# Kernel tuning notes

Measured on AMD Instinct MI355X. Metric: run time of the kernel, lower is better.

## Reference

```python
import jax, jax.numpy as jnp
import numpy as np

BB, F, K, D, H, HFF, L, M_PREV = 128, 8, 256, 256, 256, 512, 2, 2


def setup_inputs() -> dict:
    key = jax.random.key(0)
    ks = jax.random.split(key, 16)
    f32 = jnp.float32

    def lin(k, fan_in, shape):
        return (jax.random.normal(k, shape, dtype=f32) / np.sqrt(fan_in)).astype(f32)

    inp = {
        "x_BD": jax.random.normal(ks[0], (BB, D), dtype=f32),
        "xhat_BFD": jax.random.normal(ks[1], (BB, F, D), dtype=f32),
        "codes_MBF": jax.random.randint(ks[2], (M_PREV, BB, 1), 0, F * K, dtype=jnp.int64),
        "codebook": jax.random.normal(ks[3], (K, D), dtype=f32) / np.sqrt(D),
        "W_in": lin(ks[4], D, (D, H)),
        "b_in": jnp.zeros((H,), f32),
        # concat projection over cat([h, xhat], -1): (H + D) -> H
        "W_cat": lin(ks[5], H + D, (H + D, H)),
        "b_cat": jnp.zeros((H,), f32),
        "W1": lin(ks[6], H, (L, H, HFF)),
        "b1": jnp.zeros((L, HFF), f32),
        "W2": lin(ks[7], HFF, (L, HFF, H)),
        "b2": jnp.zeros((L, H), f32),
        "W_out": lin(ks[8], H, (H, D)),
        "b_out": jnp.zeros((D,), f32),
    }
    return inp


def reference(x_BD, xhat_BFD, codes_MBF, codebook, W_in, b_in, W_cat, b_cat,
              W1, b1, W2, b2, W_out, b_out):
    Bb, Fb, Dd = xhat_BFD.shape
    Kk = codebook.shape[0]

    # in_proj applied to the (shared) codebook once: [K, H]
    h0 = codebook @ W_in + b_in

    # concat(h, xhat) as a linear over the concatenation, split to avoid
    # materializing a [Bb,F,K,H+D] tensor.
    Wc, Wx = W_cat[:H], W_cat[H:]
    h = (h0 @ Wc)[None, None] + (xhat_BFD @ Wx)[:, :, None] + b_cat  # [Bb,F,K,H]

    # residual MLP blocks: h <- h + W2 relu(W1 h)
    for l in range(L):
        h = h + jax.nn.relu(h @ W1[l] + b1[l]) @ W2[l] + b2[l]

    # out_proj + residual codeword (res_codeword_coeff = 1.0) + xhat offset
    cw = h @ W_out + b_out + codebook[None, None]        # [Bb,F,K,D]
    cw = cw + xhat_BFD[:, :, None]                        # reconstructed candidates

    cflat = cw.reshape(Bb, Fb * Kk, Dd)                   # [Bb, F*K, D]

    dists = (jnp.sum(x_BD * x_BD, -1, keepdims=True)
             - 2.0 * jnp.einsum('bd,bkd->bk', x_BD, cflat)
             + jnp.sum(cflat * cflat, -1))                # [Bb, F*K]

    idx = jnp.argmin(dists, axis=-1)                      # [Bb]
    xhat_next_BFD = jnp.take_along_axis(cflat, idx[:, None, None], axis=1)  # [Bb,1,D]

    codes_new = jnp.concatenate(
        [codes_MBF, idx[None, :, None].astype(codes_MBF.dtype)], axis=0)
    return xhat_next_BFD, codes_new
```

## Files before the change

### kernel.cpp

```cpp
#include <hip/hip_runtime.h>
#include <hip/hip_bf16.h>

#define B_   128
#define F_   8
#define K_   256
#define D_   256
#define H_   256
#define HFF_ 512
#define RT   64

typedef _Float16 half8  __attribute__((ext_vector_type(8)));
typedef _Float16 half4v __attribute__((ext_vector_type(4)));
typedef float floatx4   __attribute__((ext_vector_type(4)));

#define MFMAH(a,b,c) __builtin_amdgcn_mfma_f32_16x16x32_f16(a,b,c,0,0,0)

#define HA_S  260
#define HMA_S 132

__global__ void k_prep(const float* __restrict__ cb, const float* __restrict__ Win,
                       const float* __restrict__ bin, const float* __restrict__ Wcat,
                       const float* __restrict__ bcat, const float* __restrict__ xhat,
                       const float* __restrict__ W1, const float* __restrict__ W2,
                       const float* __restrict__ Wout,
                       float* __restrict__ u, float* __restrict__ v,
                       _Float16* __restrict__ w1f, _Float16* __restrict__ w2f,
                       _Float16* __restrict__ wof) {
  const int blk = blockIdx.x, t = threadIdx.x;
  if (blk < K_) {
    __shared__ float row[D_];
    __shared__ float h0row[H_];
    row[t] = cb[blk * D_ + t];
    __syncthreads();
    float acc = bin[t];
    #pragma unroll 4
    for (int i = 0; i < D_; ++i) acc = fmaf(row[i], Win[i * H_ + t], acc);
    h0row[t] = acc;
    __syncthreads();
    float acc2 = 0.f;
    #pragma unroll 4
    for (int i = 0; i < H_; ++i) acc2 = fmaf(h0row[i], Wcat[i * H_ + t], acc2);
    u[blk * H_ + t] = acc2;
  } else if (blk < K_ + B_ * F_) {
    __shared__ float row2[D_];
    const int bf = blk - K_;
    row2[t] = xhat[bf * D_ + t];
    __syncthreads();
    float acc = bcat[t];
    #pragma unroll 4
    for (int i = 0; i < D_; ++i) acc = fmaf(row2[i], Wcat[(H_ + i) * H_ + t], acc);
    v[bf * H_ + t] = acc;
  } else {
    const int e = (blk - (K_ + B_ * F_)) * 256 + t;
    const float* src; _Float16* dst; int N, NT, le;
    if (e < 262144) {
      const int layer = e >> 17; le = e & 131071;
      src = W1 + layer * (H_ * HFF_); dst = w1f + layer * (H_ * HFF_);
      N = HFF_; NT = 32;
    } else if (e < 524288) {
      const int e2 = e - 262144;
      const int layer = e2 >> 17; le = e2 & 131071;
      src = W2 + layer * (HFF_ * H_); dst = w2f + layer * (HFF_ * H_);
      N = H_; NT = 16;
    } else {
      le = e - 524288; src = Wout; dst = wof; N = D_; NT = 16;
    }
    const int jj = le & 7, lane = (le >> 3) & 63, r = le >> 9;
    const int ntile = r % NT, kstep = r / NT;
    const int row = kstep * 32 + (lane >> 4) * 8 + jj;
    const int colc = ntile * 16 + (lane & 15);
    dst[le] = (_Float16)src[row * N + colc];
  }
}

__global__ __launch_bounds__(256, 3) void k_main(
    const float* __restrict__ u, const float* __restrict__ v,
    const _Float16* __restrict__ w1f, const float* __restrict__ b1,
    const _Float16* __restrict__ w2f, const float* __restrict__ b2,
    const _Float16* __restrict__ woutf, const float* __restrict__ bout,
    const float* __restrict__ cb, const float* __restrict__ xhat,
    const float* __restrict__ x, float* __restrict__ dists) {
  __shared__ _Float16 hA[64][HA_S];
  __shared__ _Float16 hmA[64][HMA_S];
  __shared__ float x_s[D_], xh_s[D_];
  __shared__ float dist_s[4][64];

  const int t = threadIdx.x;
  const int blk = blockIdx.x;
  const int bf = blk >> 2, k0 = (blk & 3) << 6;
  const int b = bf >> 3, f = bf & 7;
  const int wave = t >> 6, lane = t & 63;
  const int col = lane & 15, quad = lane >> 4;
  const int lane8 = lane * 8;

  x_s[t]  = x[b * D_ + t];
  xh_s[t] = xhat[bf * D_ + t];

  {
    const int r = t >> 2, c0 = (t & 3) * 64;
    const float* up = u + (k0 + r) * H_ + c0;
    const float* vp = v + bf * H_ + c0;
    #pragma unroll
    for (int j = 0; j < 64; j += 8) {
      float4 uA = *(const float4*)(up + j);
      float4 vA = *(const float4*)(vp + j);
      float4 uB = *(const float4*)(up + j + 4);
      float4 vB = *(const float4*)(vp + j + 4);
      half8 hv8;
      hv8[0] = (_Float16)(uA.x + vA.x); hv8[1] = (_Float16)(uA.y + vA.y);
      hv8[2] = (_Float16)(uA.z + vA.z); hv8[3] = (_Float16)(uA.w + vA.w);
      hv8[4] = (_Float16)(uB.x + vB.x); hv8[5] = (_Float16)(uB.y + vB.y);
      hv8[6] = (_Float16)(uB.z + vB.z); hv8[7] = (_Float16)(uB.w + vB.w);
      *(half8*)&hA[r][c0 + j] = hv8;
    }
  }
  __syncthreads();

  const floatx4 zero4 = {0.f, 0.f, 0.f, 0.f};

  #pragma unroll 1
  for (int l = 0; l < 2; ++l) {
    const _Float16* w1_l = w1f + l * (H_ * HFF_);
    const _Float16* w2_l = w2f + l * (HFF_ * H_);
    const float* b1l = b1 + l * HFF_;
    const float* b2l = b2 + l * H_;

    floatx4 acc2[4][4];
    #pragma unroll
    for (int mt = 0; mt < 4; ++mt)
      #pragma unroll
      for (int nt = 0; nt < 4; ++nt) acc2[mt][nt] = zero4;

    #pragma unroll 1
    for (int ch = 0; ch < 4; ++ch) {
      floatx4 acc1[2][4];
      #pragma unroll
      for (int mt = 0; mt < 2; ++mt)
        #pragma unroll
        for (int nt = 0; nt < 4; ++nt) acc1[mt][nt] = zero4;

      const _Float16* w1_b = w1_l + (ch * 8 + wave * 2) * 512 + lane8;

      #pragma unroll 4
      for (int ks = 0; ks < 8; ++ks) {
        half8 b0 = *(const half8*)&hA[col][ks * 32 + quad * 8];
        half8 b1v = *(const half8*)&hA[16 + col][ks * 32 + quad * 8];
        half8 b2v = *(const half8*)&hA[32 + col][ks * 32 + quad * 8];
        half8 b3v = *(const half8*)&hA[48 + col][ks * 32 + quad * 8];
        const int ko = ks * 32 * 512;
        #pragma unroll
        for (int mt = 0; mt < 2; ++mt) {
          half8 aw = *(const half8*)(w1_b + ko + mt * 512);
          acc1[mt][0] = MFMAH(aw, b0, acc1[mt][0]);
          acc1[mt][1] = MFMAH(aw, b1v, acc1[mt][1]);
          acc1[mt][2] = MFMAH(aw, b2v, acc1[mt][2]);
          acc1[mt][3] = MFMAH(aw, b3v, acc1[mt][3]);
        }
      }
      #pragma unroll
      for (int mt = 0; mt < 2; ++mt) {
        const int floc = (wave * 2 + mt) * 16 + quad * 4;
        float4 bb = *(const float4*)&b1l[ch * 128 + floc];
        #pragma unroll
        for (int nt = 0; nt < 4; ++nt) {
          const int row = nt * 16 + col;
          half4v nh;
          #pragma unroll
          for (int p = 0; p < 4; ++p)
            nh[p] = (_Float16)fmaxf(acc1[mt][nt][p] + ((const float*)&bb)[p], 0.f);
          *(half4v*)&hmA[row][floc] = nh;
        }
      }
      __syncthreads();

      const _Float16* w2_b = w2_l + (ch * 64 + wave * 4) * 512 + lane8;
      #pragma unroll 2
      for (int ks = 0; ks < 4; ++ks) {
        half8 b0 = *(const half8*)&hmA[col][ks * 32 + quad * 8];
        half8 b1v = *(const half8*)&hmA[16 + col][ks * 32 + quad * 8];
        half8 b2v = *(const half8*)&hmA[32 + col][ks * 32 + quad * 8];
        half8 b3v = *(const half8*)&hmA[48 + col][ks * 32 + quad * 8];
        const int ko = ks * 16 * 512;
        #pragma unroll
        for (int mt = 0; mt < 4; ++mt) {
          half8 aw = *(const half8*)(w2_b + ko + mt * 512);
          acc2[mt][0] = MFMAH(aw, b0, acc2[mt][0]);
          acc2[mt][1] = MFMAH(aw, b1v, acc2[mt][1]);
          acc2[mt][2] = MFMAH(aw, b2v, acc2[mt][2]);
          acc2[mt][3] = MFMAH(aw, b3v, acc2[mt][3]);
        }
      }
      __syncthreads();
    }

    #pragma unroll
    for (int mt = 0; mt < 4; ++mt) {
      const int feat0 = (wave * 4 + mt) * 16 + quad * 4;
      float4 bb = *(const float4*)&b2l[feat0];
      #pragma unroll
      for (int nt = 0; nt < 4; ++nt) {
        const int row = nt * 16 + col;
        half4v oh = *(half4v*)&hA[row][feat0];
        half4v nh;
        #pragma unroll
        for (int p = 0; p < 4; ++p)
          nh[p] = (_Float16)((float)oh[p] + acc2[mt][nt][p] + ((const float*)&bb)[p]);
        *(half4v*)&hA[row][feat0] = nh;
      }
    }
    __syncthreads();
  }

  floatx4 acc3[4][4];
  #pragma unroll
  for (int mt = 0; mt < 4; ++mt)
    #pragma unroll
    for (int nt = 0; nt < 4; ++nt) acc3[mt][nt] = zero4;

  const _Float16* wo_b = woutf + (wave * 4) * 512 + lane8;
  #pragma unroll 2
  for (int ks = 0; ks < 8; ++ks) {
    half8 b0 = *(const half8*)&hA[col][ks * 32 + quad * 8];
    half8 b1v = *(const half8*)&hA[16 + col][ks * 32 + quad * 8];
    half8 b2v = *(const half8*)&hA[32 + col][ks * 32 + quad * 8];
    half8 b3v = *(const half8*)&hA[48 + col][ks * 32 + quad * 8];
    const int ko = ks * 16 * 512;
    #pragma unroll
    for (int mt = 0; mt < 4; ++mt) {
      half8 aw = *(const half8*)(wo_b + ko + mt * 512);
      acc3[mt][0] = MFMAH(aw, b0, acc3[mt][0]);
      acc3[mt][1] = MFMAH(aw, b1v, acc3[mt][1]);
      acc3[mt][2] = MFMAH(aw, b2v, acc3[mt][2]);
      acc3[mt][3] = MFMAH(aw, b3v, acc3[mt][3]);
    }
  }

  float s[4] = {0.f, 0.f, 0.f, 0.f};
  #pragma unroll
  for (int mt = 0; mt < 4; ++mt) {
    const int d0 = (wave * 4 + mt) * 16 + quad * 4;
    float4 bo = *(const float4*)&bout[d0];
    float4 xv = *(const float4*)&x_s[d0];
    float4 xh4 = *(const float4*)&xh_s[d0];
    #pragma unroll
    for (int nt = 0; nt < 4; ++nt) {
      float4 cbv = *(const float4*)&cb[(k0 + nt * 16 + col) * D_ + d0];
      #pragma unroll
      for (int p = 0; p < 4; ++p) {
        float base = ((const float*)&bo)[p] + ((const float*)&xh4)[p];
        float xx = ((const float*)&xv)[p];
        float cw = acc3[mt][nt][p] + base + ((const float*)&cbv)[p];
        s[nt] += cw * (cw - 2.f * xx);
      }
    }
  }
  #pragma unroll
  for (int nt = 0; nt < 4; ++nt) {
    s[nt] += __shfl_xor(s[nt], 16, 64);
    s[nt] += __shfl_xor(s[nt], 32, 64);
  }
  if (quad == 0) {
    #pragma unroll
    for (int nt = 0; nt < 4; ++nt)
      dist_s[wave][nt * 16 + col] = s[nt];
  }
  __syncthreads();
  if (t < 64) {
    float d = dist_s[0][t] + dist_s[1][t] + dist_s[2][t] + dist_s[3][t];
    dists[b * (F_ * K_) + f * K_ + k0 + t] = d;
  }
}

__global__ void k_top8(const float* __restrict__ dists, int* __restrict__ topi) {
  __shared__ float ds[F_ * K_];
  __shared__ float bv[256];
  __shared__ int bi_s[256];
  const int b = blockIdx.x, t = threadIdx.x;
  for (int j = t; j < F_ * K_; j += 256) ds[j] = dists[b * (F_ * K_) + j];
  __syncthreads();
  for (int pass = 0; pass < 8; ++pass) {
    float best = 3.4e38f; int bi = 0;
    for (int j = t; j < F_ * K_; j += 256) {
      const float dv = ds[j];
      if (dv < best) { best = dv; bi = j; }
    }
    bv[t] = best; bi_s[t] = bi;
    __syncthreads();
    for (int s = 128; s > 0; s >>= 1) {
      if (t < s) {
        const float ov = bv[t + s]; const int oi = bi_s[t + s];
        if (ov < bv[t] || (ov == bv[t] && oi < bi_s[t])) { bv[t] = ov; bi_s[t] = oi; }
      }
      __syncthreads();
    }
    if (t == 0) { topi[b * 8 + pass] = bi_s[0]; ds[bi_s[0]] = 3.4e38f; }
    __syncthreads();
  }
}

__global__ void k_rescore(const float* __restrict__ u, const float* __restrict__ v,
                          const float* __restrict__ W1, const float* __restrict__ b1,
                          const float* __restrict__ W2, const float* __restrict__ b2,
                          const float* __restrict__ Wout, const float* __restrict__ bout,
                          const float* __restrict__ cb, const float* __restrict__ xhat,
                          const float* __restrict__ x, const int* __restrict__ topi,
                          float* __restrict__ resc) {
  __shared__ float hs[H_];
  __shared__ float hms[HFF_];
  __shared__ float red[256];
  const int bc = blockIdx.x, t = threadIdx.x;
  const int b = bc >> 3;
  const int idx = topi[bc];
  const int f = idx >> 8, k = idx & 255;
  const int bf = b * F_ + f;

  hs[t] = u[k * H_ + t] + v[bf * H_ + t];
  __syncthreads();
  for (int l = 0; l < 2; ++l) {
    const float* W1l = W1 + l * (H_ * HFF_);
    const float* W2l = W2 + l * (HFF_ * H_);
    float a0 = b1[l * HFF_ + t], a1 = b1[l * HFF_ + 256 + t];
    for (int i = 0; i < H_; ++i) {
      const float hv = hs[i];
      a0 = fmaf(hv, W1l[i * HFF_ + t], a0);
      a1 = fmaf(hv, W1l[i * HFF_ + 256 + t], a1);
    }
    hms[t] = fmaxf(a0, 0.f);
    hms[t + 256] = fmaxf(a1, 0.f);
    __syncthreads();
    float hn = hs[t] + b2[l * H_ + t];
    for (int jj = 0; jj < HFF_; ++jj)
      hn = fmaf(hms[jj], W2l[jj * H_ + t], hn);
    __syncthreads();
    hs[t] = hn;
    __syncthreads();
  }
  float cw = bout[t] + cb[k * D_ + t] + xhat[bf * D_ + t];
  for (int i = 0; i < H_; ++i) cw = fmaf(hs[i], Wout[i * D_ + t], cw);
  red[t] = cw * (cw - 2.f * x[b * D_ + t]);
  __syncthreads();
  for (int s = 128; s > 0; s >>= 1) {
    if (t < s) red[t] += red[t + s];
    __syncthreads();
  }
  if (t == 0) resc[bc] = red[0];
}

__global__ void k_final(const float* __restrict__ u, const float* __restrict__ v,
                        const float* __restrict__ W1, const float* __restrict__ b1,
                        const float* __restrict__ W2, const float* __restrict__ b2,
                        const float* __restrict__ Wout, const float* __restrict__ bout,
                        const float* __restrict__ cb, const float* __restrict__ xhat,
                        const int* __restrict__ codes, const int* __restrict__ topi,
                        const float* __restrict__ resc, float* __restrict__ out) {
  __shared__ float hs[H_];
  __shared__ float hms[HFF_];
  __shared__ int idx_sh;
  const int b = blockIdx.x, t = threadIdx.x;
  if (t == 0) {
    float bd = 3.4e38f; int bidx = 1 << 30;
    for (int c = 0; c < 8; ++c) {
      const float d = resc[b * 8 + c];
      const int ix = topi[b * 8 + c];
      if (d < bd || (d == bd && ix < bidx)) { bd = d; bidx = ix; }
    }
    idx_sh = bidx;
  }
  __syncthreads();
  const int idx = idx_sh;
  const int f = idx >> 8, k = idx & 255;
  const int bf = b * F_ + f;

  hs[t] = u[k * H_ + t] + v[bf * H_ + t];
  __syncthreads();
  for (int l = 0; l < 2; ++l) {
    const float* W1l = W1 + l * (H_ * HFF_);
    const float* W2l = W2 + l * (HFF_ * H_);
    float a0 = b1[l * HFF_ + t], a1 = b1[l * HFF_ + 256 + t];
    for (int i = 0; i < H_; ++i) {
      const float hv = hs[i];
      a0 = fmaf(hv, W1l[i * HFF_ + t], a0);
      a1 = fmaf(hv, W1l[i * HFF_ + 256 + t], a1);
    }
    hms[t] = fmaxf(a0, 0.f);
    hms[t + 256] = fmaxf(a1, 0.f);
    __syncthreads();
    float hn = hs[t] + b2[l * H_ + t];
    for (int jj = 0; jj < HFF_; ++jj)
      hn = fmaf(hms[jj], W2l[jj * H_ + t], hn);
    __syncthreads();
    hs[t] = hn;
    __syncthreads();
  }
  float cw = bout[t] + cb[k * D_ + t] + xhat[bf * D_ + t];
  for (int i = 0; i < H_; ++i) cw = fmaf(hs[i], Wout[i * D_ + t], cw);

  out[b * D_ + t] = cw;
  if (t < 2)
    out[B_ * D_ + t * B_ + b] = (float)codes[t * B_ + b];
  else if (t == 2)
    out[B_ * D_ + 2 * B_ + b] = (float)idx;
}

extern "C" void kernel_launch(void* const* d_in, const int* in_sizes, int n_in,
                              void* d_out, int out_size, void* d_ws, size_t ws_size,
                              hipStream_t stream) {
  const float* x    = (const float*)d_in[0];
  const float* xhat = (const float*)d_in[1];
  const int*   codes= (const int*)d_in[2];
  const float* cb   = (const float*)d_in[3];
  const float* Win  = (const float*)d_in[4];
  const float* bin  = (const float*)d_in[5];
  const float* Wcat = (const float*)d_in[6];
  const float* bcat = (const float*)d_in[7];
  const float* W1   = (const float*)d_in[8];
  const float* b1   = (const float*)d_in[9];
  const float* W2   = (const float*)d_in[10];
  const float* b2   = (const float*)d_in[11];
  const float* Wout = (const float*)d_in[12];
  const float* bout = (const float*)d_in[13];
  float* out = (float*)d_out;

  float* u     = (float*)d_ws;
  float* v     = u + K_ * H_;
  float* dists = v + B_ * F_ * H_;
  float* resc  = dists + B_ * F_ * K_;
  int*   topi  = (int*)(resc + 1024);
  int*   pad   = topi + 1024;
  _Float16* w1f  = (_Float16*)(pad + 128);
  _Float16* w2f  = w1f + 2 * H_ * HFF_;
  _Float16* wof  = w2f + 2 * HFF_ * H_;

  k_prep<<<K_ + B_ * F_ + 2304, 256, 0, stream>>>(cb, Win, bin, Wcat, bcat, xhat,
                                                  W1, W2, Wout, u, v, w1f, w2f, wof);

  k_main<<<B_ * F_ * (K_ / RT), 256, 0, stream>>>(u, v, w1f, b1, w2f, b2,
                                                  wof, bout, cb, xhat, x, dists);
  k_top8<<<B_, 256, 0, stream>>>(dists, topi);
  k_rescore<<<B_ * 8, 256, 0, stream>>>(u, v, W1, b1, W2, b2, Wout, bout, cb, xhat,
                                        x, topi, resc);
  k_final<<<B_, 256, 0, stream>>>(u, v, W1, b1, W2, b2, Wout, bout, cb, xhat,
                                  codes, topi, resc, out);
}
```

Before: 567.5 us.

## Fuse top-8 selection, fp32 rescoring and final output into one kernel

Merges the top-8 kernel, the per-candidate fp32 rescore kernel and the final recompute kernel into a single per-batch-row kernel. All 8 candidates are batched through the MLP together, so each weight load is reused for 8 FMAs. The winner's output vector is kept in registers instead of being recomputed. This removes two launches, the workspace round trips and the redundant final MLP pass. The cost is only 128 blocks doing the rescore work instead of 1024, which lowers parallelism.

```diff
diff --git a/kernel.cpp b/kernel.cpp
--- a/kernel.cpp
+++ b/kernel.cpp
@@ -271,11 +271,25 @@
   }
 }
 
-__global__ void k_top8(const float* __restrict__ dists, int* __restrict__ topi) {
+__global__ __launch_bounds__(256) void k_sel(
+    const float* __restrict__ u, const float* __restrict__ v,
+    const float* __restrict__ W1, const float* __restrict__ b1,
+    const float* __restrict__ W2, const float* __restrict__ b2,
+    const float* __restrict__ Wout, const float* __restrict__ bout,
+    const float* __restrict__ cb, const float* __restrict__ xhat,
+    const float* __restrict__ x, const int* __restrict__ codes,
+    const float* __restrict__ dists, float* __restrict__ out) {
   __shared__ float ds[F_ * K_];
+  __shared__ float hs[H_][8];
+  __shared__ float hm[HFF_][8];
   __shared__ float bv[256];
   __shared__ int bi_s[256];
+  __shared__ int topc[8];
+  __shared__ float part[4][8];
+  __shared__ int win_sh;
+
   const int b = blockIdx.x, t = threadIdx.x;
+
   for (int j = t; j < F_ * K_; j += 256) ds[j] = dists[b * (F_ * K_) + j];
   __syncthreads();
   for (int pass = 0; pass < 8; ++pass) {
@@ -293,113 +307,119 @@
       }
       __syncthreads();
     }
-    if (t == 0) { topi[b * 8 + pass] = bi_s[0]; ds[bi_s[0]] = 3.4e38f; }
-    __syncthreads();
-  }
-}
-
-__global__ void k_rescore(const float* __restrict__ u, const float* __restrict__ v,
-                          const float* __restrict__ W1, const float* __restrict__ b1,
-                          const float* __restrict__ W2, const float* __restrict__ b2,
-                          const float* __restrict__ Wout, const float* __restrict__ bout,
-                          const float* __restrict__ cb, const float* __restrict__ xhat,
-                          const float* __restrict__ x, const int* __restrict__ topi,
-                          float* __restrict__ resc) {
-  __shared__ float hs[H_];
-  __shared__ float hms[HFF_];
-  __shared__ float red[256];
-  const int bc = blockIdx.x, t = threadIdx.x;
-  const int b = bc >> 3;
-  const int idx = topi[bc];
-  const int f = idx >> 8, k = idx & 255;
-  const int bf = b * F_ + f;
-
-  hs[t] = u[k * H_ + t] + v[bf * H_ + t];
-  __syncthreads();
+    if (t == 0) { topc[pass] = bi_s[0]; ds[bi_s[0]] = 3.4e38f; }
+    __syncthreads();
+  }
+
+  int kc[8], bfc[8];
+  #pragma unroll
+  for (int c = 0; c < 8; ++c) {
+    const int idx = topc[c];
+    kc[c] = idx & 255;
+    bfc[c] = b * F_ + (idx >> 8);
+  }
+
+  #pragma unroll
+  for (int c = 0; c < 8; ++c)
+    hs[t][c] = u[kc[c] * H_ + t] + v[bfc[c] * H_ + t];
+  __syncthreads();
+
   for (int l = 0; l < 2; ++l) {
     const float* W1l = W1 + l * (H_ * HFF_);
     const float* W2l = W2 + l * (HFF_ * H_);
-    float a0 = b1[l * HFF_ + t], a1 = b1[l * HFF_ + 256 + t];
+    float a0[8], a1[8];
+    {
+      const float bb0 = b1[l * HFF_ + t], bb1 = b1[l * HFF_ + 256 + t];
+      #pragma unroll
+      for (int c = 0; c < 8; ++c) { a0[c] = bb0; a1[c] = bb1; }
+    }
+    #pragma unroll 4
     for (int i = 0; i < H_; ++i) {
-      const float hv = hs[i];
-      a0 = fmaf(hv, W1l[i * HFF_ + t], a0);
-      a1 = fmaf(hv, W1l[i * HFF_ + 256 + t], a1);
-    }
-    hms[t] = fmaxf(a0, 0.f);
-    hms[t + 256] = fmaxf(a1, 0.f);
-    __syncthreads();
-    float hn = hs[t] + b2[l * H_ + t];
-    for (int jj = 0; jj < HFF_; ++jj)
-      hn = fmaf(hms[jj], W2l[jj * H_ + t], hn);
-    __syncthreads();
-    hs[t] = hn;
-    __syncthreads();
-  }
-  float cw = bout[t] + cb[k * D_ + t] + xhat[bf * D_ + t];
-  for (int i = 0; i < H_; ++i) cw = fmaf(hs[i], Wout[i * D_ + t], cw);
-  red[t] = cw * (cw - 2.f * x[b * D_ + t]);
-  __syncthreads();
-  for (int s = 128; s > 0; s >>= 1) {
-    if (t < s) red[t] += red[t + s];
-    __syncthreads();
-  }
-  if (t == 0) resc[bc] = red[0];
-}
-
-__global__ void k_final(const float* __restrict__ u, const float* __restrict__ v,
-                        const float* __restrict__ W1, const float* __restrict__ b1,
-                        const float* __restrict__ W2, const float* __restrict__ b2,
-                        const float* __restrict__ Wout, const float* __restrict__ bout,
-                        const float* __restrict__ cb, const float* __restrict__ xhat,
-                        const int* __restrict__ codes, const int* __restrict__ topi,
-                        const float* __restrict__ resc, float* __restrict__ out) {
-  __shared__ float hs[H_];
-  __shared__ float hms[HFF_];
-  __shared__ int idx_sh;
-  const int b = blockIdx.x, t = threadIdx.x;
+      const float w0 = W1l[i * HFF_ + t];
+      const float w1 = W1l[i * HFF_ + 256 + t];
+      float hv[8];
+      *(float4*)&hv[0] = *(const float4*)&hs[i][0];
+      *(float4*)&hv[4] = *(const float4*)&hs[i][4];
+      #pragma unroll
+      for (int c = 0; c < 8; ++c) {
+        a0[c] = fmaf(hv[c], w0, a0[c]);
+        a1[c] = fmaf(hv[c], w1, a1[c]);
+      }
+    }
+    #pragma unroll
+    for (int c = 0; c < 8; ++c) {
+      hm[t][c] = fmaxf(a0[c], 0.f);
+      hm[t + 256][c] = fmaxf(a1[c], 0.f);
+    }
+    __syncthreads();
+
+    float hn[8];
+    {
+      const float bb = b2[l * H_ + t];
+      #pragma unroll
+      for (int c = 0; c < 8; ++c) hn[c] = hs[t][c] + bb;
+    }
+    #pragma unroll 4
+    for (int jj = 0; jj < HFF_; ++jj) {
+      const float w = W2l[jj * H_ + t];
+      float hv[8];
+      *(float4*)&hv[0] = *(const float4*)&hm[jj][0];
+      *(float4*)&hv[4] = *(const float4*)&hm[jj][4];
+      #pragma unroll
+      for (int c = 0; c < 8; ++c) hn[c] = fmaf(hv[c], w, hn[c]);
+    }
+    #pragma unroll
+    for (int c = 0; c < 8; ++c) hs[t][c] = hn[c];
+    __syncthreads();
+  }
+
+  float cw[8];
+  #pragma unroll
+  for (int c = 0; c < 8; ++c)
+    cw[c] = bout[t] + cb[kc[c] * D_ + t] + xhat[bfc[c] * D_ + t];
+  #pragma unroll 4
+  for (int i = 0; i < H_; ++i) {
+    const float w = Wout[i * D_ + t];
+    float hv[8];
+    *(float4*)&hv[0] = *(const float4*)&hs[i][0];
+    *(float4*)&hv[4] = *(const float4*)&hs[i][4];
+    #pragma unroll
+    for (int c = 0; c < 8; ++c) cw[c] = fmaf(hv[c], w, cw[c]);
+  }
+
+  const float xx = x[b * D_ + t];
+  float rd[8];
+  #pragma unroll
+  for (int c = 0; c < 8; ++c) rd[c] = cw[c] * (cw[c] - 2.f * xx);
+  #pragma unroll
+  for (int m = 1; m < 64; m <<= 1)
+    #pragma unroll
+    for (int c = 0; c < 8; ++c) rd[c] += __shfl_xor(rd[c], m, 64);
+  const int wave = t >> 6, lane = t & 63;
+  if (lane == 0) {
+    #pragma unroll
+    for (int c = 0; c < 8; ++c) part[wave][c] = rd[c];
+  }
+  __syncthreads();
   if (t == 0) {
-    float bd = 3.4e38f; int bidx = 1 << 30;
+    float bd = 3.4e38f; int bwin = 0; int bidx = 1 << 30;
     for (int c = 0; c < 8; ++c) {
-      const float d = resc[b * 8 + c];
-      const int ix = topi[b * 8 + c];
-      if (d < bd || (d == bd && ix < bidx)) { bd = d; bidx = ix; }
-    }
-    idx_sh = bidx;
-  }
-  __syncthreads();
-  const int idx = idx_sh;
-  const int f = idx >> 8, k = idx & 255;
-  const int bf = b * F_ + f;
-
-  hs[t] = u[k * H_ + t] + v[bf * H_ + t];
-  __syncthreads();
-  for (int l = 0; l < 2; ++l) {
-    const float* W1l = W1 + l * (H_ * HFF_);
-    const float* W2l = W2 + l * (HFF_ * H_);
-    float a0 = b1[l * HFF_ + t], a1 = b1[l * HFF_ + 256 + t];
-    for (int i = 0; i < H_; ++i) {
-      const float hv = hs[i];
-      a0 = fmaf(hv, W1l[i * HFF_ + t], a0);
-      a1 = fmaf(hv, W1l[i * HFF_ + 256 + t], a1);
-    }
-    hms[t] = fmaxf(a0, 0.f);
-    hms[t + 256] = fmaxf(a1, 0.f);
-    __syncthreads();
-    float hn = hs[t] + b2[l * H_ + t];
-    for (int jj = 0; jj < HFF_; ++jj)
-      hn = fmaf(hms[jj], W2l[jj * H_ + t], hn);
-    __syncthreads();
-    hs[t] = hn;
-    __syncthreads();
-  }
-  float cw = bout[t] + cb[k * D_ + t] + xhat[bf * D_ + t];
-  for (int i = 0; i < H_; ++i) cw = fmaf(hs[i], Wout[i * D_ + t], cw);
-
-  out[b * D_ + t] = cw;
+      const float d = part[0][c] + part[1][c] + part[2][c] + part[3][c];
+      const int ix = topc[c];
+      if (d < bd || (d == bd && ix < bidx)) { bd = d; bwin = c; bidx = ix; }
+    }
+    win_sh = bwin;
+  }
+  __syncthreads();
+  const int win = win_sh;
+  float cwsel = cw[0];
+  #pragma unroll
+  for (int c = 1; c < 8; ++c) cwsel = (win == c) ? cw[c] : cwsel;
+  out[b * D_ + t] = cwsel;
   if (t < 2)
     out[B_ * D_ + t * B_ + b] = (float)codes[t * B_ + b];
   else if (t == 2)
-    out[B_ * D_ + 2 * B_ + b] = (float)idx;
+    out[B_ * D_ + 2 * B_ + b] = (float)topc[win];
 }
 
 extern "C" void kernel_launch(void* const* d_in, const int* in_sizes, int n_in,
@@ -424,10 +444,8 @@
   float* u     = (float*)d_ws;
   float* v     = u + K_ * H_;
   float* dists = v + B_ * F_ * H_;
-  float* resc  = dists + B_ * F_ * K_;
-  int*   topi  = (int*)(resc + 1024);
-  int*   pad   = topi + 1024;
-  _Float16* w1f  = (_Float16*)(pad + 128);
+  float* pad   = dists + B_ * F_ * K_;
+  _Float16* w1f  = (_Float16*)(pad + 256);
   _Float16* w2f  = w1f + 2 * H_ * HFF_;
   _Float16* wof  = w2f + 2 * HFF_ * H_;
 
@@ -436,9 +454,7 @@
 
   k_main<<<B_ * F_ * (K_ / RT), 256, 0, stream>>>(u, v, w1f, b1, w2f, b2,
                                                   wof, bout, cb, xhat, x, dists);
-  k_top8<<<B_, 256, 0, stream>>>(dists, topi);
-  k_rescore<<<B_ * 8, 256, 0, stream>>>(u, v, W1, b1, W2, b2, Wout, bout, cb, xhat,
-                                        x, topi, resc);
-  k_final<<<B_, 256, 0, stream>>>(u, v, W1, b1, W2, b2, Wout, bout, cb, xhat,
-                                  codes, topi, resc, out);
+
+  k_sel<<<B_, 256, 0, stream>>>(u, v, W1, b1, W2, b2, Wout, bout, cb, xhat,
+                                x, codes, dists, out);
 }
```

Result: slower. 591.8 us (+4.3%).

## Cache rescored candidates and process two candidates per rescore block

Applied to the files above, without the earlier changes.

The rescore kernel now evaluates two top-8 candidates per block, sharing each weight load between them, and halves the grid. It writes each candidate's reconstructed vector to workspace. The final kernel then copies the winning vector instead of recomputing the full fp32 MLP chain. This removes a redundant serial MLP pass and halves weight traffic in rescoring, at the cost of fewer blocks and extra workspace.

```diff
diff --git a/kernel.cpp b/kernel.cpp
--- a/kernel.cpp
+++ b/kernel.cpp
@@ -298,108 +298,100 @@
   }
 }
 
-__global__ void k_rescore(const float* __restrict__ u, const float* __restrict__ v,
-                          const float* __restrict__ W1, const float* __restrict__ b1,
-                          const float* __restrict__ W2, const float* __restrict__ b2,
-                          const float* __restrict__ Wout, const float* __restrict__ bout,
-                          const float* __restrict__ cb, const float* __restrict__ xhat,
-                          const float* __restrict__ x, const int* __restrict__ topi,
-                          float* __restrict__ resc) {
-  __shared__ float hs[H_];
-  __shared__ float hms[HFF_];
-  __shared__ float red[256];
-  const int bc = blockIdx.x, t = threadIdx.x;
-  const int b = bc >> 3;
-  const int idx = topi[bc];
-  const int f = idx >> 8, k = idx & 255;
-  const int bf = b * F_ + f;
-
-  hs[t] = u[k * H_ + t] + v[bf * H_ + t];
+__global__ __launch_bounds__(256) void k_rescore(
+    const float* __restrict__ u, const float* __restrict__ v,
+    const float* __restrict__ W1, const float* __restrict__ b1,
+    const float* __restrict__ W2, const float* __restrict__ b2,
+    const float* __restrict__ Wout, const float* __restrict__ bout,
+    const float* __restrict__ cb, const float* __restrict__ xhat,
+    const float* __restrict__ x, const int* __restrict__ topi,
+    float* __restrict__ resc, float* __restrict__ cwr) {
+  __shared__ float hsA[H_], hsB[H_];
+  __shared__ float hmA2[HFF_], hmB2[HFF_];
+  __shared__ float redA[256], redB[256];
+  const int blk = blockIdx.x, t = threadIdx.x;
+  const int b = blk >> 2;
+  const int c0 = (blk & 3) * 2;
+  const int bcA = b * 8 + c0, bcB = bcA + 1;
+  const int idxA = topi[bcA], idxB = topi[bcB];
+  const int kA = idxA & 255, kB = idxB & 255;
+  const int bfA = b * F_ + (idxA >> 8), bfB = b * F_ + (idxB >> 8);
+
+  hsA[t] = u[kA * H_ + t] + v[bfA * H_ + t];
+  hsB[t] = u[kB * H_ + t] + v[bfB * H_ + t];
   __syncthreads();
   for (int l = 0; l < 2; ++l) {
     const float* W1l = W1 + l * (H_ * HFF_);
     const float* W2l = W2 + l * (HFF_ * H_);
-    float a0 = b1[l * HFF_ + t], a1 = b1[l * HFF_ + 256 + t];
+    const float bb0 = b1[l * HFF_ + t], bb1 = b1[l * HFF_ + 256 + t];
+    float a0A = bb0, a1A = bb1, a0B = bb0, a1B = bb1;
+    #pragma unroll 4
     for (int i = 0; i < H_; ++i) {
-      const float hv = hs[i];
-      a0 = fmaf(hv, W1l[i * HFF_ + t], a0);
-      a1 = fmaf(hv, W1l[i * HFF_ + 256 + t], a1);
-    }
-    hms[t] = fmaxf(a0, 0.f);
-    hms[t + 256] = fmaxf(a1, 0.f);
-    __syncthreads();
-    float hn = hs[t] + b2[l * H_ + t];
-    for (int jj = 0; jj < HFF_; ++jj)
-      hn = fmaf(hms[jj], W2l[jj * H_ + t], hn);
-    __syncthreads();
-    hs[t] = hn;
-    __syncthreads();
-  }
-  float cw = bout[t] + cb[k * D_ + t] + xhat[bf * D_ + t];
-  for (int i = 0; i < H_; ++i) cw = fmaf(hs[i], Wout[i * D_ + t], cw);
-  red[t] = cw * (cw - 2.f * x[b * D_ + t]);
+      const float w0 = W1l[i * HFF_ + t];
+      const float w1 = W1l[i * HFF_ + 256 + t];
+      const float hA = hsA[i], hB = hsB[i];
+      a0A = fmaf(hA, w0, a0A);
+      a1A = fmaf(hA, w1, a1A);
+      a0B = fmaf(hB, w0, a0B);
+      a1B = fmaf(hB, w1, a1B);
+    }
+    hmA2[t] = fmaxf(a0A, 0.f);  hmA2[t + 256] = fmaxf(a1A, 0.f);
+    hmB2[t] = fmaxf(a0B, 0.f);  hmB2[t + 256] = fmaxf(a1B, 0.f);
+    __syncthreads();
+    const float bb2 = b2[l * H_ + t];
+    float hnA = hsA[t] + bb2, hnB = hsB[t] + bb2;
+    #pragma unroll 4
+    for (int jj = 0; jj < HFF_; ++jj) {
+      const float w = W2l[jj * H_ + t];
+      hnA = fmaf(hmA2[jj], w, hnA);
+      hnB = fmaf(hmB2[jj], w, hnB);
+    }
+    __syncthreads();
+    hsA[t] = hnA; hsB[t] = hnB;
+    __syncthreads();
+  }
+  float cwA = bout[t] + cb[kA * D_ + t] + xhat[bfA * D_ + t];
+  float cwB = bout[t] + cb[kB * D_ + t] + xhat[bfB * D_ + t];
+  #pragma unroll 4
+  for (int i = 0; i < H_; ++i) {
+    const float w = Wout[i * D_ + t];
+    cwA = fmaf(hsA[i], w, cwA);
+    cwB = fmaf(hsB[i], w, cwB);
+  }
+  cwr[bcA * D_ + t] = cwA;
+  cwr[bcB * D_ + t] = cwB;
+  const float xx = x[b * D_ + t];
+  redA[t] = cwA * (cwA - 2.f * xx);
+  redB[t] = cwB * (cwB - 2.f * xx);
   __syncthreads();
   for (int s = 128; s > 0; s >>= 1) {
-    if (t < s) red[t] += red[t + s];
-    __syncthreads();
-  }
-  if (t == 0) resc[bc] = red[0];
-}
-
-__global__ void k_final(const float* __restrict__ u, const float* __restrict__ v,
-                        const float* __restrict__ W1, const float* __restrict__ b1,
-                        const float* __restrict__ W2, const float* __restrict__ b2,
-                        const float* __restrict__ Wout, const float* __restrict__ bout,
-                        const float* __restrict__ cb, const float* __restrict__ xhat,
-                        const int* __restrict__ codes, const int* __restrict__ topi,
-                        const float* __restrict__ resc, float* __restrict__ out) {
-  __shared__ float hs[H_];
-  __shared__ float hms[HFF_];
-  __shared__ int idx_sh;
+    if (t < s) { redA[t] += redA[t + s]; redB[t] += redB[t + s]; }
+    __syncthreads();
+  }
+  if (t == 0) { resc[bcA] = redA[0]; resc[bcB] = redB[0]; }
+}
+
+__global__ void k_final(const int* __restrict__ codes, const int* __restrict__ topi,
+                        const float* __restrict__ resc, const float* __restrict__ cwr,
+                        float* __restrict__ out) {
+  __shared__ int win_sh;
   const int b = blockIdx.x, t = threadIdx.x;
   if (t == 0) {
-    float bd = 3.4e38f; int bidx = 1 << 30;
+    float bd = 3.4e38f; int bwin = 0; int bidx = 1 << 30;
     for (int c = 0; c < 8; ++c) {
       const float d = resc[b * 8 + c];
       const int ix = topi[b * 8 + c];
-      if (d < bd || (d == bd && ix < bidx)) { bd = d; bidx = ix; }
-    }
-    idx_sh = bidx;
-  }
-  __syncthreads();
-  const int idx = idx_sh;
-  const int f = idx >> 8, k = idx & 255;
-  const int bf = b * F_ + f;
-
-  hs[t] = u[k * H_ + t] + v[bf * H_ + t];
-  __syncthreads();
-  for (int l = 0; l < 2; ++l) {
-    const float* W1l = W1 + l * (H_ * HFF_);
-    const float* W2l = W2 + l * (HFF_ * H_);
-    float a0 = b1[l * HFF_ + t], a1 = b1[l * HFF_ + 256 + t];
-    for (int i = 0; i < H_; ++i) {
-      const float hv = hs[i];
-      a0 = fmaf(hv, W1l[i * HFF_ + t], a0);
-      a1 = fmaf(hv, W1l[i * HFF_ + 256 + t], a1);
-    }
-    hms[t] = fmaxf(a0, 0.f);
-    hms[t + 256] = fmaxf(a1, 0.f);
-    __syncthreads();
-    float hn = hs[t] + b2[l * H_ + t];
-    for (int jj = 0; jj < HFF_; ++jj)
-      hn = fmaf(hms[jj], W2l[jj * H_ + t], hn);
-    __syncthreads();
-    hs[t] = hn;
-    __syncthreads();
-  }
-  float cw = bout[t] + cb[k * D_ + t] + xhat[bf * D_ + t];
-  for (int i = 0; i < H_; ++i) cw = fmaf(hs[i], Wout[i * D_ + t], cw);
-
-  out[b * D_ + t] = cw;
+      if (d < bd || (d == bd && ix < bidx)) { bd = d; bwin = c; bidx = ix; }
+    }
+    win_sh = bwin;
+  }
+  __syncthreads();
+  const int win = win_sh;
+  out[b * D_ + t] = cwr[(b * 8 + win) * D_ + t];
   if (t < 2)
     out[B_ * D_ + t * B_ + b] = (float)codes[t * B_ + b];
   else if (t == 2)
-    out[B_ * D_ + 2 * B_ + b] = (float)idx;
+    out[B_ * D_ + 2 * B_ + b] = (float)topi[b * 8 + win];
 }
 
 extern "C" void kernel_launch(void* const* d_in, const int* in_sizes, int n_in,
@@ -426,7 +418,8 @@
   float* dists = v + B_ * F_ * H_;
   float* resc  = dists + B_ * F_ * K_;
   int*   topi  = (int*)(resc + 1024);
-  int*   pad   = topi + 1024;
+  float* cwr   = (float*)(topi + 1024);
+  float* pad   = cwr + B_ * 8 * D_;
   _Float16* w1f  = (_Float16*)(pad + 128);
   _Float16* w2f  = w1f + 2 * H_ * HFF_;
   _Float16* wof  = w2f + 2 * HFF_ * H_;
@@ -436,9 +429,9 @@
 
   k_main<<<B_ * F_ * (K_ / RT), 256, 0, stream>>>(u, v, w1f, b1, w2f, b2,
                                                   wof, bout, cb, xhat, x, dists);
+
   k_top8<<<B_, 256, 0, stream>>>(dists, topi);
-  k_rescore<<<B_ * 8, 256, 0, stream>>>(u, v, W1, b1, W2, b2, Wout, bout, cb, xhat,
-                                        x, topi, resc);
-  k_final<<<B_, 256, 0, stream>>>(u, v, W1, b1, W2, b2, Wout, bout, cb, xhat,
-                                  codes, topi, resc, out);
-}
+  k_rescore<<<B_ * 4, 256, 0, stream>>>(u, v, W1, b1, W2, b2, Wout, bout, cb, xhat,
+                                        x, topi, resc, cwr);
+  k_final<<<B_, 256, 0, stream>>>(codes, topi, resc, cwr, out);
+}
```

After: 590.6 us. 1.04x slower.
